# Kernel optimization log

Hardware: AMD Instinct MI355X
Metric: run time of the kernel (lower is better)

Reference implementation:

```python
import jax, jax.numpy as jnp
import numpy as np
import math

EMBED_DIM = 1024
NUM_HEADS = 16
HEAD_DIM = EMBED_DIM // NUM_HEADS
B, S = 4, 2048


def setup_inputs() -> dict:
    key = jax.random.key(0)
    ks = jax.random.split(key, 9)
    scale = 1.0 / math.sqrt(EMBED_DIM)
    def lin(k):
        kw, kb = jax.random.split(k)
        W = jax.random.uniform(kw, (EMBED_DIM, EMBED_DIM), jnp.float32, -scale, scale)
        b = jax.random.uniform(kb, (EMBED_DIM,), jnp.float32, -scale, scale)
        return W, b
    Wq, bq = lin(ks[0]); Wk, bk = lin(ks[1]); Wv, bv = lin(ks[2]); Wo, bo = lin(ks[3])
    x = jax.random.normal(ks[4], (B, S, EMBED_DIM), jnp.float32)
    return {"x": x, "Wq": Wq, "bq": bq, "Wk": Wk, "bk": bk,
            "Wv": Wv, "bv": bv, "Wo": Wo, "bo": bo}


def reference(x, Wq, bq, Wk, bk, Wv, bv, Wo, bo):
    Bx, Sx, E = x.shape
    def proj(W, b):
        y = jnp.einsum('bse,oe->bso', x, W) + b
        return y.reshape(Bx, Sx, NUM_HEADS, HEAD_DIM).transpose(0, 2, 1, 3)  # [B,H,S,D]
    q = proj(Wq, bq)
    k = proj(Wk, bk)
    v = proj(Wv, bv)
    scores = jnp.einsum('bhsd,bhtd->bhst', q, k) / math.sqrt(HEAD_DIM)
    # causal mask (paged_cache is None, seq_len > 1)
    causal = jnp.tril(jnp.ones((Sx, Sx), dtype=bool))
    scores = jnp.where(causal[None, None], scores, -jnp.inf)
    attn = jax.nn.softmax(scores, axis=-1)
    out = jnp.einsum('bhst,bhtd->bhsd', attn, v)
    out = out.transpose(0, 2, 1, 3).reshape(Bx, Sx, E)
    return jnp.einsum('bse,oe->bso', out, Wo) + bo
```

## Files before the change

kernel.cpp:

```cpp
#include <hip/hip_runtime.h>
#include <hip/hip_bf16.h>
#include <stdint.h>

#define EDIM 1024
#define NH   16
#define HD   64
#define BB   4
#define SS   2048
#define MROWS (BB*SS)

typedef __bf16 bf16x8 __attribute__((ext_vector_type(8)));
typedef __bf16 bf16x4 __attribute__((ext_vector_type(4)));
typedef float  f32x4  __attribute__((ext_vector_type(4)));
typedef float  f32x16 __attribute__((ext_vector_type(16)));
typedef int    int2v  __attribute__((ext_vector_type(2)));

__device__ __forceinline__ void async16(const void* g, void* lds) {
    __builtin_amdgcn_global_load_lds((__attribute__((address_space(1))) void*)(g),
                                     (__attribute__((address_space(3))) void*)(lds),
                                     16, 0, 0);
}

__device__ __forceinline__ f32x4 mfma16(bf16x8 a, bf16x8 b, f32x4 c) {
    return __builtin_amdgcn_mfma_f32_16x16x32_bf16(a, b, c, 0, 0, 0);
}
__device__ __forceinline__ f32x16 mfma32(bf16x8 a, bf16x8 b, f32x16 c) {
    return __builtin_amdgcn_mfma_f32_32x32x16_bf16(a, b, c, 0, 0, 0);
}

__device__ __forceinline__ int pkbf16(float a, float b) {
    union { __bf16 h[2]; int i; } u;
    u.h[0] = (__bf16)a; u.h[1] = (__bf16)b;
    return u.i;
}

__global__ __launch_bounds__(256) void cvt_kernel(const float* __restrict__ s,
                                                  __bf16* __restrict__ d, int n) {
    int i = (blockIdx.x * 256 + threadIdx.x) * 4;
    if (i < n) {
        float4 v = *reinterpret_cast<const float4*>(s + i);
        bf16x4 o;
        o.x = (__bf16)v.x; o.y = (__bf16)v.y; o.z = (__bf16)v.z; o.w = (__bf16)v.w;
        *reinterpret_cast<bf16x4*>(d + i) = o;
    }
}

__global__ __launch_bounds__(256) void gemm_qkv(const __bf16* __restrict__ A,
                                                const __bf16* __restrict__ W,
                                                const float* __restrict__ bq,
                                                const float* __restrict__ bk,
                                                const float* __restrict__ bv,
                                                __bf16* __restrict__ Qb,
                                                __bf16* __restrict__ Kb,
                                                __bf16* __restrict__ Vtb) {
    __shared__ char As[128 * 64];
    __shared__ char Bs[128 * 64];

    const int tid = threadIdx.x;
    const int w = tid >> 6, l = tid & 63;
    const int bm = blockIdx.x * 128, bn = blockIdx.y * 128;
    const int wm = (w >> 1) * 64, wn = (w & 1) * 64;

    f32x4 acc[4][4] = {};
    const int lrow = l & 15;
    const int lslot = l >> 4;

    for (int kt = 0; kt < EDIM / 32; ++kt) {
        const int k0 = kt * 32;
        #pragma unroll
        for (int i = 0; i < 2; ++i) {
            int c = i * 256 + tid;
            int row = c >> 2, cb = c & 3;
            int gk = k0 + ((cb ^ (row & 3)) << 3);
            async16(A + (size_t)(bm + row) * EDIM + gk, As + (i * 256 + w * 64) * 16);
            async16(W + (size_t)(bn + row) * EDIM + gk, Bs + (i * 256 + w * 64) * 16);
        }
        __syncthreads();

        bf16x8 af[4], bfr[4];
        #pragma unroll
        for (int mf = 0; mf < 4; ++mf) {
            int row = wm + mf * 16 + lrow;
            af[mf] = *reinterpret_cast<const bf16x8*>(As + row * 64 + ((lslot ^ (row & 3)) << 4));
        }
        #pragma unroll
        for (int nf = 0; nf < 4; ++nf) {
            int row = wn + nf * 16 + lrow;
            bfr[nf] = *reinterpret_cast<const bf16x8*>(Bs + row * 64 + ((lslot ^ (row & 3)) << 4));
        }
        #pragma unroll
        for (int mf = 0; mf < 4; ++mf)
            #pragma unroll
            for (int nf = 0; nf < 4; ++nf)
                acc[mf][nf] = mfma16(af[mf], bfr[nf], acc[mf][nf]);
        __syncthreads();
    }

    const int mat = bn >> 10;
    const float* bias = (mat == 0) ? bq : (mat == 1) ? bk : bv;
    __bf16* qk = (mat == 0) ? Qb : Kb;

    #pragma unroll
    for (int nf = 0; nf < 4; ++nf) {
        int ng = bn + wn + nf * 16 + lrow;
        int nn = ng & 1023;
        int h = nn >> 6, d = nn & 63;
        float bval = bias[nn];
        #pragma unroll
        for (int mf = 0; mf < 4; ++mf) {
            #pragma unroll
            for (int r = 0; r < 4; ++r) {
                int mg = bm + wm + mf * 16 + (l >> 4) * 4 + r;
                float v = acc[mf][nf][r] + bval;
                int b = mg >> 11, s = mg & 2047;
                if (mat == 2)
                    Vtb[((size_t)(b * NH + h) * HD + d) * SS + s] = (__bf16)v;
                else
                    qk[((size_t)(b * NH + h) * SS + s) * HD + d] = (__bf16)v;
            }
        }
    }
}

__global__ __launch_bounds__(256) void gemm_out(const __bf16* __restrict__ A,
                                                const __bf16* __restrict__ W,
                                                const float* __restrict__ bias,
                                                float* __restrict__ dst) {
    __shared__ char As[128 * 64];
    __shared__ char Bs[128 * 64];

    const int tid = threadIdx.x;
    const int w = tid >> 6, l = tid & 63;
    const int bm = blockIdx.x * 128, bn = blockIdx.y * 128;
    const int wm = (w >> 1) * 64, wn = (w & 1) * 64;

    f32x4 acc[4][4] = {};
    const int lrow = l & 15;
    const int lslot = l >> 4;

    for (int kt = 0; kt < EDIM / 32; ++kt) {
        const int k0 = kt * 32;
        #pragma unroll
        for (int i = 0; i < 2; ++i) {
            int c = i * 256 + tid;
            int row = c >> 2, cb = c & 3;
            int gk = k0 + ((cb ^ (row & 3)) << 3);
            async16(A + (size_t)(bm + row) * EDIM + gk, As + (i * 256 + w * 64) * 16);
            async16(W + (size_t)(bn + row) * EDIM + gk, Bs + (i * 256 + w * 64) * 16);
        }
        __syncthreads();

        bf16x8 af[4], bfr[4];
        #pragma unroll
        for (int mf = 0; mf < 4; ++mf) {
            int row = wm + mf * 16 + lrow;
            af[mf] = *reinterpret_cast<const bf16x8*>(As + row * 64 + ((lslot ^ (row & 3)) << 4));
        }
        #pragma unroll
        for (int nf = 0; nf < 4; ++nf) {
            int row = wn + nf * 16 + lrow;
            bfr[nf] = *reinterpret_cast<const bf16x8*>(Bs + row * 64 + ((lslot ^ (row & 3)) << 4));
        }
        #pragma unroll
        for (int mf = 0; mf < 4; ++mf)
            #pragma unroll
            for (int nf = 0; nf < 4; ++nf)
                acc[mf][nf] = mfma16(af[mf], bfr[nf], acc[mf][nf]);
        __syncthreads();
    }

    #pragma unroll
    for (int nf = 0; nf < 4; ++nf) {
        int ng = bn + wn + nf * 16 + lrow;
        float bval = bias[ng];
        #pragma unroll
        for (int mf = 0; mf < 4; ++mf) {
            #pragma unroll
            for (int r = 0; r < 4; ++r) {
                int mg = bm + wm + mf * 16 + (l >> 4) * 4 + r;
                dst[(size_t)mg * EDIM + ng] = acc[mf][nf][r] + bval;
            }
        }
    }
}

#define SCL2E 0.18033688f

__global__ __launch_bounds__(512) void attn_kernel(const __bf16* __restrict__ Q,
                                                   const __bf16* __restrict__ K,
                                                   const __bf16* __restrict__ Vt,
                                                   __bf16* __restrict__ Oa) {
    __shared__ char ks0[64 * 128], vs0[64 * 128];
    __shared__ char ks1[64 * 128], vs1[64 * 128];

    const int bh = blockIdx.x;
    const int qt = 7 - blockIdx.y;
    const int tid = threadIdx.x;
    const int w = tid >> 6;
    const int l = tid & 63;
    const int lo = l & 31;
    const int hi = l >> 5;

    const __bf16* Qp = Q + (size_t)bh * (SS * HD);
    const __bf16* Kp = K + (size_t)bh * (SS * HD);
    const __bf16* Vp = Vt + (size_t)bh * (HD * SS);

    const int qg = qt * 256 + w * 32 + lo;
    bf16x8 qf[4];
    #pragma unroll
    for (int kc = 0; kc < 4; ++kc)
        qf[kc] = *reinterpret_cast<const bf16x8*>(Qp + (size_t)qg * HD + kc * 16 + hi * 8);

    const int rowS = tid >> 3, cbS = tid & 7;
    const int gsS = (cbS ^ (rowS & 7)) << 3;
    const int wb = w * 1024;
    const __bf16* kp = Kp + (size_t)rowS * HD + gsS;
    const __bf16* vp = Vp + (size_t)rowS * SS + gsS;

    f32x16 oacc[2] = {};
    float mrow = -1e30f;
    float lsum = 0.f;

    const int qwhi = qt * 256 + w * 32 + 31;
    const int ntiles = 4 * qt + 4;

    auto compute = [&](const char* ksb, const char* vsb, int kv0) {
        f32x16 acc[2] = {};
        __builtin_amdgcn_s_setprio(1);
        #pragma unroll
        for (int tb = 0; tb < 2; ++tb) {
            const int t = tb * 32 + lo;
            const char* krow = ksb + t * 128;
            const int tx = (t & 7);
            #pragma unroll
            for (int kc = 0; kc < 4; ++kc) {
                bf16x8 kf = *reinterpret_cast<const bf16x8*>(krow + ((2 * kc + hi) ^ tx) * 16);
                acc[tb] = mfma32(kf, qf[kc], acc[tb]);
            }
        }
        __builtin_amdgcn_s_setprio(0);

        if (kv0 + 63 > qg - lo) {
            #pragma unroll
            for (int tb = 0; tb < 2; ++tb)
                #pragma unroll
                for (int r = 0; r < 16; ++r) {
                    int t = kv0 + tb * 32 + ((r & 3) + 8 * (r >> 2)) + 4 * hi;
                    if (t > qg) acc[tb][r] = -1e30f;
                }
        }

        float mx = acc[0][0];
        #pragma unroll
        for (int r = 1; r < 16; ++r) mx = fmaxf(mx, acc[0][r]);
        #pragma unroll
        for (int r = 0; r < 16; ++r) mx = fmaxf(mx, acc[1][r]);
        mx = fmaxf(mx, __shfl_xor(mx, 32));
        float mxs = mx * SCL2E;
        if (!__all(mxs <= mrow + 8.0f)) {
            float mnew = fmaxf(mrow, mxs);
            float alpha = exp2f(mrow - mnew);
            mrow = mnew;
            lsum *= alpha;
            oacc[0] *= alpha;
            oacc[1] *= alpha;
        }
        float psum = 0.f;
        #pragma unroll
        for (int tb = 0; tb < 2; ++tb)
            #pragma unroll
            for (int r = 0; r < 16; ++r) {
                float p = exp2f(fmaf(acc[tb][r], SCL2E, -mrow));
                acc[tb][r] = p;
                psum += p;
            }
        lsum += psum;

        bf16x8 pa[4];
        #pragma unroll
        for (int ks2 = 0; ks2 < 4; ++ks2) {
            const int tb = ks2 >> 1, rb = (ks2 & 1) * 8;
            int a0 = pkbf16(acc[tb][rb + 0], acc[tb][rb + 1]);
            int b0 = pkbf16(acc[tb][rb + 4], acc[tb][rb + 5]);
            int a1 = pkbf16(acc[tb][rb + 2], acc[tb][rb + 3]);
            int b1 = pkbf16(acc[tb][rb + 6], acc[tb][rb + 7]);
            int2v s1 = __builtin_amdgcn_permlane32_swap(a0, b0, false, false);
            int2v s2 = __builtin_amdgcn_permlane32_swap(a1, b1, false, false);
            union { int i[4]; bf16x8 v; } u;
            u.i[0] = s1[0]; u.i[1] = s2[0]; u.i[2] = s1[1]; u.i[3] = s2[1];
            pa[ks2] = u.v;
        }

        __builtin_amdgcn_s_setprio(1);
        #pragma unroll
        for (int ks2 = 0; ks2 < 4; ++ks2) {
            #pragma unroll
            for (int db = 0; db < 2; ++db) {
                const int d = db * 32 + lo;
                bf16x8 vb = *reinterpret_cast<const bf16x8*>(
                    vsb + d * 128 + (((2 * ks2 + hi) ^ (d & 7)) * 16));
                oacc[db] = mfma32(vb, pa[ks2], oacc[db]);
            }
        }
        __builtin_amdgcn_s_setprio(0);
    };

    async16(kp, ks0 + wb);
    async16(vp, vs0 + wb);
    kp += 64 * HD; vp += 64;

    for (int kt = 0; kt < ntiles; kt += 2) {
        async16(kp, ks1 + wb);
        async16(vp, vs1 + wb);
        kp += 64 * HD; vp += 64;
        asm volatile("s_waitcnt vmcnt(2)" ::: "memory");
        __builtin_amdgcn_s_barrier();
        __builtin_amdgcn_sched_barrier(0);
        if (kt * 64 <= qwhi) compute(ks0, vs0, kt * 64);
        __builtin_amdgcn_sched_barrier(0);
        __builtin_amdgcn_s_barrier();

        if (kt + 2 < ntiles) {
            async16(kp, ks0 + wb);
            async16(vp, vs0 + wb);
            kp += 64 * HD; vp += 64;
            asm volatile("s_waitcnt vmcnt(2)" ::: "memory");
        } else {
            asm volatile("s_waitcnt vmcnt(0)" ::: "memory");
        }
        __builtin_amdgcn_s_barrier();
        __builtin_amdgcn_sched_barrier(0);
        if ((kt + 1) * 64 <= qwhi) compute(ks1, vs1, (kt + 1) * 64);
        __builtin_amdgcn_sched_barrier(0);
        __builtin_amdgcn_s_barrier();
    }

    const int b = bh >> 4, h = bh & 15;
    float lsumt = lsum + __shfl_xor(lsum, 32);
    float inv = 1.0f / lsumt;
    __bf16* orow = Oa + ((size_t)(b * SS + qg)) * EDIM + h * HD;
    #pragma unroll
    for (int db = 0; db < 2; ++db) {
        #pragma unroll
        for (int g = 0; g < 4; ++g) {
            int d0 = db * 32 + g * 8 + 4 * hi;
            bf16x4 o4;
            o4.x = (__bf16)(oacc[db][g * 4 + 0] * inv);
            o4.y = (__bf16)(oacc[db][g * 4 + 1] * inv);
            o4.z = (__bf16)(oacc[db][g * 4 + 2] * inv);
            o4.w = (__bf16)(oacc[db][g * 4 + 3] * inv);
            *reinterpret_cast<bf16x4*>(orow + d0) = o4;
        }
    }
}

extern "C" void kernel_launch(void* const* d_in, const int* in_sizes, int n_in,
                              void* d_out, int out_size, void* d_ws, size_t ws_size,
                              hipStream_t stream) {
    const float* x  = (const float*)d_in[0];
    const float* Wq = (const float*)d_in[1];
    const float* bq = (const float*)d_in[2];
    const float* Wk = (const float*)d_in[3];
    const float* bk = (const float*)d_in[4];
    const float* Wv = (const float*)d_in[5];
    const float* bv = (const float*)d_in[6];
    const float* Wo = (const float*)d_in[7];
    const float* bo = (const float*)d_in[8];

    char* ws = (char*)d_ws;
    const size_t SZ_XB  = (size_t)MROWS * EDIM * 2;
    const size_t SZ_W   = (size_t)EDIM * EDIM * 2;
    const size_t SZ_QKV = (size_t)BB * NH * SS * HD * 2;

    __bf16* xb  = (__bf16*)(ws);
    __bf16* wqb = (__bf16*)(ws + SZ_XB);
    __bf16* wkb = (__bf16*)(ws + SZ_XB + SZ_W);
    __bf16* wvb = (__bf16*)(ws + SZ_XB + 2 * SZ_W);
    __bf16* wob = (__bf16*)(ws + SZ_XB + 3 * SZ_W);
    __bf16* Qb  = (__bf16*)(ws + SZ_XB + 4 * SZ_W);
    __bf16* Kb  = (__bf16*)(ws + SZ_XB + 4 * SZ_W + SZ_QKV);
    __bf16* Vtb = (__bf16*)(ws + SZ_XB + 4 * SZ_W + 2 * SZ_QKV);
    __bf16* Oab = (__bf16*)(ws + SZ_XB + 4 * SZ_W + 3 * SZ_QKV);

    cvt_kernel<<<MROWS * EDIM / 1024, 256, 0, stream>>>(x, xb, MROWS * EDIM);
    cvt_kernel<<<EDIM * EDIM / 1024, 256, 0, stream>>>(Wq, wqb, EDIM * EDIM);
    cvt_kernel<<<EDIM * EDIM / 1024, 256, 0, stream>>>(Wk, wkb, EDIM * EDIM);
    cvt_kernel<<<EDIM * EDIM / 1024, 256, 0, stream>>>(Wv, wvb, EDIM * EDIM);
    cvt_kernel<<<EDIM * EDIM / 1024, 256, 0, stream>>>(Wo, wob, EDIM * EDIM);

    gemm_qkv<<<dim3(MROWS / 128, 3 * EDIM / 128), 256, 0, stream>>>(
        xb, wqb, bq, bk, bv, Qb, Kb, Vtb);

    attn_kernel<<<dim3(BB * NH, 8), 512, 0, stream>>>(Qb, Kb, Vtb, Oab);

    gemm_out<<<dim3(MROWS / 128, EDIM / 128), 256, 0, stream>>>(
        Oab, wob, bo, (float*)d_out);
}
```

Measured before the change: 215.6 us.

## Process KV tiles in pairs to overlap softmax with next QK MFMA

Restructures the attention main loop to stage two 64-key tiles per buffer and run them as a pair: the QK product for the second tile is issued before the PV product for the first, then the softmax of the second tile runs. This software pipelining lets MFMA work interleave with the exp/max VALU work and halves the number of barriers per key. LDS use doubles to 64KB and launch_bounds adds a min-blocks hint of 4, which raises register pressure from holding two accumulator sets and may reduce occupancy.

```diff
diff --git a/kernel.cpp b/kernel.cpp
--- a/kernel.cpp
+++ b/kernel.cpp
@@ -186,12 +186,12 @@
 
 #define SCL2E 0.18033688f
 
-__global__ __launch_bounds__(512) void attn_kernel(const __bf16* __restrict__ Q,
-                                                   const __bf16* __restrict__ K,
-                                                   const __bf16* __restrict__ Vt,
-                                                   __bf16* __restrict__ Oa) {
-    __shared__ char ks0[64 * 128], vs0[64 * 128];
-    __shared__ char ks1[64 * 128], vs1[64 * 128];
+__global__ __launch_bounds__(512, 4) void attn_kernel(const __bf16* __restrict__ Q,
+                                                      const __bf16* __restrict__ K,
+                                                      const __bf16* __restrict__ Vt,
+                                                      __bf16* __restrict__ Oa) {
+    __shared__ char kP0[2][64 * 128], vP0[2][64 * 128];
+    __shared__ char kP1[2][64 * 128], vP1[2][64 * 128];
 
     const int bh = blockIdx.x;
     const int qt = 7 - blockIdx.y;
@@ -222,10 +222,9 @@
     float lsum = 0.f;
 
     const int qwhi = qt * 256 + w * 32 + 31;
-    const int ntiles = 4 * qt + 4;
-
-    auto compute = [&](const char* ksb, const char* vsb, int kv0) {
-        f32x16 acc[2] = {};
+    const int nquads = qt + 1;
+
+    auto qk = [&](const char* ksb, f32x16 acc[2]) {
         __builtin_amdgcn_s_setprio(1);
         #pragma unroll
         for (int tb = 0; tb < 2; ++tb) {
@@ -239,7 +238,9 @@
             }
         }
         __builtin_amdgcn_s_setprio(0);
-
+    };
+
+    auto smpa = [&](f32x16 acc[2], int kv0, bf16x8 pa[4]) {
         if (kv0 + 63 > qg - lo) {
             #pragma unroll
             for (int tb = 0; tb < 2; ++tb)
@@ -249,7 +250,6 @@
                     if (t > qg) acc[tb][r] = -1e30f;
                 }
         }
-
         float mx = acc[0][0];
         #pragma unroll
         for (int r = 1; r < 16; ++r) mx = fmaxf(mx, acc[0][r]);
@@ -275,8 +275,6 @@
                 psum += p;
             }
         lsum += psum;
-
-        bf16x8 pa[4];
         #pragma unroll
         for (int ks2 = 0; ks2 < 4; ++ks2) {
             const int tb = ks2 >> 1, rb = (ks2 & 1) * 8;
@@ -290,7 +288,9 @@
             u.i[0] = s1[0]; u.i[1] = s2[0]; u.i[2] = s1[1]; u.i[3] = s2[1];
             pa[ks2] = u.v;
         }
-
+    };
+
+    auto pv = [&](const char* vsb, bf16x8 pa[4]) {
         __builtin_amdgcn_s_setprio(1);
         #pragma unroll
         for (int ks2 = 0; ks2 < 4; ++ks2) {
@@ -305,32 +305,52 @@
         __builtin_amdgcn_s_setprio(0);
     };
 
-    async16(kp, ks0 + wb);
-    async16(vp, vs0 + wb);
-    kp += 64 * HD; vp += 64;
-
-    for (int kt = 0; kt < ntiles; kt += 2) {
-        async16(kp, ks1 + wb);
-        async16(vp, vs1 + wb);
+    auto pair = [&](const char kb[2][64 * 128], const char vb[2][64 * 128], int kv0) {
+        if (kv0 > qwhi) return;
+        f32x16 accA[2] = {};
+        qk(kb[0], accA);
+        bf16x8 paA[4];
+        smpa(accA, kv0, paA);
+        const bool doB = (kv0 + 64) <= qwhi;
+        if (doB) {
+            f32x16 accB[2] = {};
+            qk(kb[1], accB);
+            pv(vb[0], paA);
+            bf16x8 paB[4];
+            smpa(accB, kv0 + 64, paB);
+            pv(vb[1], paB);
+        } else {
+            pv(vb[0], paA);
+        }
+    };
+
+    auto stage = [&](char kb[2][64 * 128], char vb[2][64 * 128]) {
+        async16(kp, kb[0] + wb); async16(vp, vb[0] + wb);
         kp += 64 * HD; vp += 64;
-        asm volatile("s_waitcnt vmcnt(2)" ::: "memory");
+        async16(kp, kb[1] + wb); async16(vp, vb[1] + wb);
+        kp += 64 * HD; vp += 64;
+    };
+
+    stage(kP0, vP0);
+
+    for (int q = 0; q < nquads; ++q) {
+        stage(kP1, vP1);
+        asm volatile("s_waitcnt vmcnt(4)" ::: "memory");
         __builtin_amdgcn_s_barrier();
         __builtin_amdgcn_sched_barrier(0);
-        if (kt * 64 <= qwhi) compute(ks0, vs0, kt * 64);
+        pair(kP0, vP0, q * 256);
         __builtin_amdgcn_sched_barrier(0);
         __builtin_amdgcn_s_barrier();
 
-        if (kt + 2 < ntiles) {
-            async16(kp, ks0 + wb);
-            async16(vp, vs0 + wb);
-            kp += 64 * HD; vp += 64;
-            asm volatile("s_waitcnt vmcnt(2)" ::: "memory");
+        if (q + 1 < nquads) {
+            stage(kP0, vP0);
+            asm volatile("s_waitcnt vmcnt(4)" ::: "memory");
         } else {
             asm volatile("s_waitcnt vmcnt(0)" ::: "memory");
         }
         __builtin_amdgcn_s_barrier();
         __builtin_amdgcn_sched_barrier(0);
-        if ((kt + 1) * 64 <= qwhi) compute(ks1, vs1, (kt + 1) * 64);
+        pair(kP1, vP1, q * 256 + 128);
         __builtin_amdgcn_sched_barrier(0);
         __builtin_amdgcn_s_barrier();
     }
```

New measurement: 218.6 us. No clear change (+1.4%).

## Shrink attention query tile to 128 rows and merge weight conversions into one launch

Applied to the files above, without the earlier changes.

The attention kernel moves from 512-thread blocks covering 256 query rows to 256-thread blocks covering 128 rows, doubling the grid. To keep the 64-row K/V tile staging intact with half the threads, each wave now issues two async loads per buffer, and the wait counts are adjusted to match. The four separate weight fp32-to-bf16 conversion launches are also fused into a single kernel that writes contiguous outputs. The smaller attention blocks aim to improve occupancy and load balance across the causal triangle, at the cost of more K/V reloads per head.

```diff
diff --git a/kernel.cpp b/kernel.cpp
--- a/kernel.cpp
+++ b/kernel.cpp
@@ -43,6 +43,20 @@
         o.x = (__bf16)v.x; o.y = (__bf16)v.y; o.z = (__bf16)v.z; o.w = (__bf16)v.w;
         *reinterpret_cast<bf16x4*>(d + i) = o;
     }
+}
+
+__global__ __launch_bounds__(256) void cvt4_kernel(const float* __restrict__ s0,
+                                                   const float* __restrict__ s1,
+                                                   const float* __restrict__ s2,
+                                                   const float* __restrict__ s3,
+                                                   __bf16* __restrict__ d) {
+    int m = blockIdx.x >> 10;
+    const float* s = (m == 0) ? s0 : (m == 1) ? s1 : (m == 2) ? s2 : s3;
+    int i = ((blockIdx.x & 1023) * 256 + threadIdx.x) * 4;
+    float4 v = *reinterpret_cast<const float4*>(s + i);
+    bf16x4 o;
+    o.x = (__bf16)v.x; o.y = (__bf16)v.y; o.z = (__bf16)v.z; o.w = (__bf16)v.w;
+    *reinterpret_cast<bf16x4*>(d + (size_t)m * (EDIM * EDIM) + i) = o;
 }
 
 __global__ __launch_bounds__(256) void gemm_qkv(const __bf16* __restrict__ A,
@@ -186,7 +200,7 @@
 
 #define SCL2E 0.18033688f
 
-__global__ __launch_bounds__(512) void attn_kernel(const __bf16* __restrict__ Q,
+__global__ __launch_bounds__(256) void attn_kernel(const __bf16* __restrict__ Q,
                                                    const __bf16* __restrict__ K,
                                                    const __bf16* __restrict__ Vt,
                                                    __bf16* __restrict__ Oa) {
@@ -194,7 +208,7 @@
     __shared__ char ks1[64 * 128], vs1[64 * 128];
 
     const int bh = blockIdx.x;
-    const int qt = 7 - blockIdx.y;
+    const int qt = 15 - blockIdx.y;
     const int tid = threadIdx.x;
     const int w = tid >> 6;
     const int l = tid & 63;
@@ -205,7 +219,7 @@
     const __bf16* Kp = K + (size_t)bh * (SS * HD);
     const __bf16* Vp = Vt + (size_t)bh * (HD * SS);
 
-    const int qg = qt * 256 + w * 32 + lo;
+    const int qg = qt * 128 + w * 32 + lo;
     bf16x8 qf[4];
     #pragma unroll
     for (int kc = 0; kc < 4; ++kc)
@@ -221,8 +235,8 @@
     float mrow = -1e30f;
     float lsum = 0.f;
 
-    const int qwhi = qt * 256 + w * 32 + 31;
-    const int ntiles = 4 * qt + 4;
+    const int qwhi = qt * 128 + w * 32 + 31;
+    const int ntiles = 2 * qt + 2;
 
     auto compute = [&](const char* ksb, const char* vsb, int kv0) {
         f32x16 acc[2] = {};
@@ -305,15 +319,19 @@
         __builtin_amdgcn_s_setprio(0);
     };
 
-    async16(kp, ks0 + wb);
-    async16(vp, vs0 + wb);
-    kp += 64 * HD; vp += 64;
+    auto stage = [&](char* kb, char* vb) {
+        async16(kp, kb + wb);
+        async16(kp + 32 * HD, kb + 4096 + wb);
+        async16(vp, vb + wb);
+        async16(vp + 32 * SS, vb + 4096 + wb);
+        kp += 64 * HD; vp += 64;
+    };
+
+    stage(ks0, vs0);
 
     for (int kt = 0; kt < ntiles; kt += 2) {
-        async16(kp, ks1 + wb);
-        async16(vp, vs1 + wb);
-        kp += 64 * HD; vp += 64;
-        asm volatile("s_waitcnt vmcnt(2)" ::: "memory");
+        stage(ks1, vs1);
+        asm volatile("s_waitcnt vmcnt(4)" ::: "memory");
         __builtin_amdgcn_s_barrier();
         __builtin_amdgcn_sched_barrier(0);
         if (kt * 64 <= qwhi) compute(ks0, vs0, kt * 64);
@@ -321,10 +339,8 @@
         __builtin_amdgcn_s_barrier();
 
         if (kt + 2 < ntiles) {
-            async16(kp, ks0 + wb);
-            async16(vp, vs0 + wb);
-            kp += 64 * HD; vp += 64;
-            asm volatile("s_waitcnt vmcnt(2)" ::: "memory");
+            stage(ks0, vs0);
+            asm volatile("s_waitcnt vmcnt(4)" ::: "memory");
         } else {
             asm volatile("s_waitcnt vmcnt(0)" ::: "memory");
         }
@@ -374,8 +390,6 @@
 
     __bf16* xb  = (__bf16*)(ws);
     __bf16* wqb = (__bf16*)(ws + SZ_XB);
-    __bf16* wkb = (__bf16*)(ws + SZ_XB + SZ_W);
-    __bf16* wvb = (__bf16*)(ws + SZ_XB + 2 * SZ_W);
     __bf16* wob = (__bf16*)(ws + SZ_XB + 3 * SZ_W);
     __bf16* Qb  = (__bf16*)(ws + SZ_XB + 4 * SZ_W);
     __bf16* Kb  = (__bf16*)(ws + SZ_XB + 4 * SZ_W + SZ_QKV);
@@ -383,15 +397,12 @@
     __bf16* Oab = (__bf16*)(ws + SZ_XB + 4 * SZ_W + 3 * SZ_QKV);
 
     cvt_kernel<<<MROWS * EDIM / 1024, 256, 0, stream>>>(x, xb, MROWS * EDIM);
-    cvt_kernel<<<EDIM * EDIM / 1024, 256, 0, stream>>>(Wq, wqb, EDIM * EDIM);
-    cvt_kernel<<<EDIM * EDIM / 1024, 256, 0, stream>>>(Wk, wkb, EDIM * EDIM);
-    cvt_kernel<<<EDIM * EDIM / 1024, 256, 0, stream>>>(Wv, wvb, EDIM * EDIM);
-    cvt_kernel<<<EDIM * EDIM / 1024, 256, 0, stream>>>(Wo, wob, EDIM * EDIM);
+    cvt4_kernel<<<4096, 256, 0, stream>>>(Wq, Wk, Wv, Wo, wqb);
 
     gemm_qkv<<<dim3(MROWS / 128, 3 * EDIM / 128), 256, 0, stream>>>(
         xb, wqb, bq, bk, bv, Qb, Kb, Vtb);
 
-    attn_kernel<<<dim3(BB * NH, 8), 512, 0, stream>>>(Qb, Kb, Vtb, Oab);
+    attn_kernel<<<dim3(BB * NH, SS / 128), 256, 0, stream>>>(Qb, Kb, Vtb, Oab);
 
     gemm_out<<<dim3(MROWS / 128, EDIM / 128), 256, 0, stream>>>(
         Oab, wob, bo, (float*)d_out);
```

Result: no change. 211.6 us (-1.9%).

## Double-buffer LDS in projection GEMMs and merge weight conversion launches

Applied to the files above, without the earlier changes.

Both projection GEMMs now use two LDS buffers, so the next K-tile's async global-to-LDS loads are issued while the current tile is computed. Partial vmcnt waits with raw barriers and sched_barriers enforce ordering, and MFMA sections run at raised wave priority. The four weight fp32-to-bf16 conversions are merged into one launch to cut launch overhead. LDS use per block doubles, which may reduce occupancy, and the hand-written waitcnt logic is fragile.

```diff
diff --git a/kernel.cpp b/kernel.cpp
--- a/kernel.cpp
+++ b/kernel.cpp
@@ -45,6 +45,97 @@
     }
 }
 
+__global__ __launch_bounds__(256) void cvt4_kernel(const float* __restrict__ s0,
+                                                   const float* __restrict__ s1,
+                                                   const float* __restrict__ s2,
+                                                   const float* __restrict__ s3,
+                                                   __bf16* __restrict__ d) {
+    int m = blockIdx.x >> 10;
+    const float* s = (m == 0) ? s0 : (m == 1) ? s1 : (m == 2) ? s2 : s3;
+    int i = ((blockIdx.x & 1023) * 256 + threadIdx.x) * 4;
+    float4 v = *reinterpret_cast<const float4*>(s + i);
+    bf16x4 o;
+    o.x = (__bf16)v.x; o.y = (__bf16)v.y; o.z = (__bf16)v.z; o.w = (__bf16)v.w;
+    *reinterpret_cast<bf16x4*>(d + (size_t)m * (EDIM * EDIM) + i) = o;
+}
+
+struct GemmCtx {
+    const __bf16 *ap0, *ap1, *bp0, *bp1;
+    int wb0, wb1;
+};
+
+__device__ __forceinline__ void g_stage(GemmCtx& c, char* As, char* Bs) {
+    async16(c.ap0, As + c.wb0);
+    async16(c.ap1, As + c.wb1);
+    async16(c.bp0, Bs + c.wb0);
+    async16(c.bp1, Bs + c.wb1);
+    c.ap0 += 32; c.ap1 += 32; c.bp0 += 32; c.bp1 += 32;
+}
+
+__device__ __forceinline__ void g_compute(const char* As, const char* Bs,
+                                          int wm, int wn, int lrow, int lslot,
+                                          f32x4 acc[4][4]) {
+    bf16x8 af[4], bfr[4];
+    #pragma unroll
+    for (int mf = 0; mf < 4; ++mf) {
+        int row = wm + mf * 16 + lrow;
+        af[mf] = *reinterpret_cast<const bf16x8*>(As + row * 64 + ((lslot ^ (row & 3)) << 4));
+    }
+    #pragma unroll
+    for (int nf = 0; nf < 4; ++nf) {
+        int row = wn + nf * 16 + lrow;
+        bfr[nf] = *reinterpret_cast<const bf16x8*>(Bs + row * 64 + ((lslot ^ (row & 3)) << 4));
+    }
+    __builtin_amdgcn_s_setprio(1);
+    #pragma unroll
+    for (int mf = 0; mf < 4; ++mf)
+        #pragma unroll
+        for (int nf = 0; nf < 4; ++nf)
+            acc[mf][nf] = mfma16(af[mf], bfr[nf], acc[mf][nf]);
+    __builtin_amdgcn_s_setprio(0);
+}
+
+#define GEMM_DBUF_LOOP()                                                      \
+    g_stage(ctx, As0, Bs0);                                                   \
+    for (int kt = 0; kt < 32; kt += 2) {                                      \
+        g_stage(ctx, As1, Bs1);                                               \
+        asm volatile("s_waitcnt vmcnt(4)" ::: "memory");                      \
+        __builtin_amdgcn_s_barrier();                                         \
+        __builtin_amdgcn_sched_barrier(0);                                    \
+        g_compute(As0, Bs0, wm, wn, lrow, lslot, acc);                        \
+        __builtin_amdgcn_sched_barrier(0);                                    \
+        __builtin_amdgcn_s_barrier();                                         \
+        if (kt + 2 < 32) {                                                    \
+            g_stage(ctx, As0, Bs0);                                           \
+            asm volatile("s_waitcnt vmcnt(4)" ::: "memory");                  \
+        } else {                                                              \
+            asm volatile("s_waitcnt vmcnt(0)" ::: "memory");                  \
+        }                                                                     \
+        __builtin_amdgcn_s_barrier();                                         \
+        __builtin_amdgcn_sched_barrier(0);                                    \
+        g_compute(As1, Bs1, wm, wn, lrow, lslot, acc);                        \
+        __builtin_amdgcn_sched_barrier(0);                                    \
+        __builtin_amdgcn_s_barrier();                                         \
+    }
+
+#define GEMM_PREAMBLE(Aptr, Wptr)                                             \
+    const int tid = threadIdx.x;                                              \
+    const int w = tid >> 6, l = tid & 63;                                     \
+    const int bm = blockIdx.x * 128, bn = blockIdx.y * 128;                   \
+    const int wm = (w >> 1) * 64, wn = (w & 1) * 64;                          \
+    f32x4 acc[4][4] = {};                                                     \
+    const int lrow = l & 15;                                                  \
+    const int lslot = l >> 4;                                                 \
+    const int row0 = tid >> 2, cb0 = tid & 3;                                 \
+    const int row1 = 64 + row0;                                               \
+    GemmCtx ctx;                                                              \
+    ctx.ap0 = (Aptr) + (size_t)(bm + row0) * EDIM + ((cb0 ^ (row0 & 3)) << 3);\
+    ctx.ap1 = (Aptr) + (size_t)(bm + row1) * EDIM + ((cb0 ^ (row1 & 3)) << 3);\
+    ctx.bp0 = (Wptr) + (size_t)(bn + row0) * EDIM + ((cb0 ^ (row0 & 3)) << 3);\
+    ctx.bp1 = (Wptr) + (size_t)(bn + row1) * EDIM + ((cb0 ^ (row1 & 3)) << 3);\
+    ctx.wb0 = (w * 64) * 16;                                                  \
+    ctx.wb1 = (256 + w * 64) * 16;
+
 __global__ __launch_bounds__(256) void gemm_qkv(const __bf16* __restrict__ A,
                                                 const __bf16* __restrict__ W,
                                                 const float* __restrict__ bq,
@@ -53,48 +144,10 @@
                                                 __bf16* __restrict__ Qb,
                                                 __bf16* __restrict__ Kb,
                                                 __bf16* __restrict__ Vtb) {
-    __shared__ char As[128 * 64];
-    __shared__ char Bs[128 * 64];
-
-    const int tid = threadIdx.x;
-    const int w = tid >> 6, l = tid & 63;
-    const int bm = blockIdx.x * 128, bn = blockIdx.y * 128;
-    const int wm = (w >> 1) * 64, wn = (w & 1) * 64;
-
-    f32x4 acc[4][4] = {};
-    const int lrow = l & 15;
-    const int lslot = l >> 4;
-
-    for (int kt = 0; kt < EDIM / 32; ++kt) {
-        const int k0 = kt * 32;
-        #pragma unroll
-        for (int i = 0; i < 2; ++i) {
-            int c = i * 256 + tid;
-            int row = c >> 2, cb = c & 3;
-            int gk = k0 + ((cb ^ (row & 3)) << 3);
-            async16(A + (size_t)(bm + row) * EDIM + gk, As + (i * 256 + w * 64) * 16);
-            async16(W + (size_t)(bn + row) * EDIM + gk, Bs + (i * 256 + w * 64) * 16);
-        }
-        __syncthreads();
-
-        bf16x8 af[4], bfr[4];
-        #pragma unroll
-        for (int mf = 0; mf < 4; ++mf) {
-            int row = wm + mf * 16 + lrow;
-            af[mf] = *reinterpret_cast<const bf16x8*>(As + row * 64 + ((lslot ^ (row & 3)) << 4));
-        }
-        #pragma unroll
-        for (int nf = 0; nf < 4; ++nf) {
-            int row = wn + nf * 16 + lrow;
-            bfr[nf] = *reinterpret_cast<const bf16x8*>(Bs + row * 64 + ((lslot ^ (row & 3)) << 4));
-        }
-        #pragma unroll
-        for (int mf = 0; mf < 4; ++mf)
-            #pragma unroll
-            for (int nf = 0; nf < 4; ++nf)
-                acc[mf][nf] = mfma16(af[mf], bfr[nf], acc[mf][nf]);
-        __syncthreads();
-    }
+    __shared__ char As0[128 * 64], Bs0[128 * 64];
+    __shared__ char As1[128 * 64], Bs1[128 * 64];
+    GEMM_PREAMBLE(A, W)
+    GEMM_DBUF_LOOP()
 
     const int mat = bn >> 10;
     const float* bias = (mat == 0) ? bq : (mat == 1) ? bk : bv;
@@ -126,48 +179,10 @@
                                                 const __bf16* __restrict__ W,
                                                 const float* __restrict__ bias,
                                                 float* __restrict__ dst) {
-    __shared__ char As[128 * 64];
-    __shared__ char Bs[128 * 64];
-
-    const int tid = threadIdx.x;
-    const int w = tid >> 6, l = tid & 63;
-    const int bm = blockIdx.x * 128, bn = blockIdx.y * 128;
-    const int wm = (w >> 1) * 64, wn = (w & 1) * 64;
-
-    f32x4 acc[4][4] = {};
-    const int lrow = l & 15;
-    const int lslot = l >> 4;
-
-    for (int kt = 0; kt < EDIM / 32; ++kt) {
-        const int k0 = kt * 32;
-        #pragma unroll
-        for (int i = 0; i < 2; ++i) {
-            int c = i * 256 + tid;
-            int row = c >> 2, cb = c & 3;
-            int gk = k0 + ((cb ^ (row & 3)) << 3);
-            async16(A + (size_t)(bm + row) * EDIM + gk, As + (i * 256 + w * 64) * 16);
-            async16(W + (size_t)(bn + row) * EDIM + gk, Bs + (i * 256 + w * 64) * 16);
-        }
-        __syncthreads();
-
-        bf16x8 af[4], bfr[4];
-        #pragma unroll
-        for (int mf = 0; mf < 4; ++mf) {
-            int row = wm + mf * 16 + lrow;
-            af[mf] = *reinterpret_cast<const bf16x8*>(As + row * 64 + ((lslot ^ (row & 3)) << 4));
-        }
-        #pragma unroll
-        for (int nf = 0; nf < 4; ++nf) {
-            int row = wn + nf * 16 + lrow;
-            bfr[nf] = *reinterpret_cast<const bf16x8*>(Bs + row * 64 + ((lslot ^ (row & 3)) << 4));
-        }
-        #pragma unroll
-        for (int mf = 0; mf < 4; ++mf)
-            #pragma unroll
-            for (int nf = 0; nf < 4; ++nf)
-                acc[mf][nf] = mfma16(af[mf], bfr[nf], acc[mf][nf]);
-        __syncthreads();
-    }
+    __shared__ char As0[128 * 64], Bs0[128 * 64];
+    __shared__ char As1[128 * 64], Bs1[128 * 64];
+    GEMM_PREAMBLE(A, W)
+    GEMM_DBUF_LOOP()
 
     #pragma unroll
     for (int nf = 0; nf < 4; ++nf) {
@@ -374,8 +389,6 @@
 
     __bf16* xb  = (__bf16*)(ws);
     __bf16* wqb = (__bf16*)(ws + SZ_XB);
-    __bf16* wkb = (__bf16*)(ws + SZ_XB + SZ_W);
-    __bf16* wvb = (__bf16*)(ws + SZ_XB + 2 * SZ_W);
     __bf16* wob = (__bf16*)(ws + SZ_XB + 3 * SZ_W);
     __bf16* Qb  = (__bf16*)(ws + SZ_XB + 4 * SZ_W);
     __bf16* Kb  = (__bf16*)(ws + SZ_XB + 4 * SZ_W + SZ_QKV);
@@ -383,10 +396,7 @@
     __bf16* Oab = (__bf16*)(ws + SZ_XB + 4 * SZ_W + 3 * SZ_QKV);
 
     cvt_kernel<<<MROWS * EDIM / 1024, 256, 0, stream>>>(x, xb, MROWS * EDIM);
-    cvt_kernel<<<EDIM * EDIM / 1024, 256, 0, stream>>>(Wq, wqb, EDIM * EDIM);
-    cvt_kernel<<<EDIM * EDIM / 1024, 256, 0, stream>>>(Wk, wkb, EDIM * EDIM);
-    cvt_kernel<<<EDIM * EDIM / 1024, 256, 0, stream>>>(Wv, wvb, EDIM * EDIM);
-    cvt_kernel<<<EDIM * EDIM / 1024, 256, 0, stream>>>(Wo, wob, EDIM * EDIM);
+    cvt4_kernel<<<4096, 256, 0, stream>>>(Wq, Wk, Wv, Wo, wqb);
 
     gemm_qkv<<<dim3(MROWS / 128, 3 * EDIM / 128), 256, 0, stream>>>(
         xb, wqb, bq, bk, bv, Qb, Kb, Vtb);
```

Result: faster. 203.2 us (-5.8%).
